# Optimization experiments

Hardware: AMD Instinct MI355X
Metric: run time of the kernel (lower is better)

The kernel has to match this reference:

```python
import jax, jax.numpy as jnp
import numpy as np
from jax import lax

WINDOW_SIZE = 11
SIGMA = 1.5
C1 = 0.01 ** 2
C2 = 0.03 ** 2


def _gaussian_window(channel, window_size, sigma=SIGMA):
    x = jnp.arange(window_size, dtype=jnp.float32)
    g = jnp.exp(-((x - window_size // 2) ** 2) / (2.0 * sigma * sigma))
    g = g / g.sum()
    w2d = jnp.outer(g, g)  # [ws, ws]
    # depthwise kernel in OIHW with feature_group_count=channel: [C, 1, ws, ws]
    return jnp.broadcast_to(w2d[None, None], (channel, 1, window_size, window_size))


def _dwconv(x, window, pad, channel):
    return lax.conv_general_dilated(
        x, window, window_strides=(1, 1), padding=[(pad, pad), (pad, pad)],
        dimension_numbers=("NCHW", "OIHW", "NCHW"), feature_group_count=channel)


def setup_inputs() -> dict:
    key = jax.random.key(0)
    k1, k2 = jax.random.split(key)
    shape = (16, 3, 512, 512)
    img1 = jax.random.uniform(k1, shape, dtype=jnp.float32)
    img2 = jax.random.uniform(k2, shape, dtype=jnp.float32)
    return {"img1": img1, "img2": img2}


def reference(img1, img2):
    _, channel, height, width = img1.shape
    ws = min(WINDOW_SIZE, height, width)
    window = _gaussian_window(channel, ws).astype(img1.dtype)
    pad = WINDOW_SIZE // 2  # matches torch code: padding=window_size // 2

    mu1 = _dwconv(img1, window, pad, channel)
    mu2 = _dwconv(img2, window, pad, channel)
    mu1_sq = mu1 * mu1
    mu2_sq = mu2 * mu2
    mu1_mu2 = mu1 * mu2

    sigma1_sq = _dwconv(img1 * img1, window, pad, channel) - mu1_sq
    sigma2_sq = _dwconv(img2 * img2, window, pad, channel) - mu2_sq
    sigma12 = _dwconv(img1 * img2, window, pad, channel) - mu1_mu2

    ssim_map = ((2.0 * mu1_mu2 + C1) * (2.0 * sigma12 + C2)) / (
        (mu1_sq + mu2_sq + C1) * (sigma1_sq + sigma2_sq + C2))
    return 1.0 - ssim_map.mean()
```

## Files before the change

### kernel.cpp

```cpp
#include <hip/hip_runtime.h>
#include <hip/hip_fp16.h>


#define IMGH 512
#define IMGW 512
#define TW 64
#define TH 32
#define GX 8
#define GY 16
#define GZ 48
#define NBLOCKS (GX * GY * GZ)
#define NPIX (16 * 3 * 512 * 512)
#define C1F 1.0e-4f
#define C2F 9.0e-4f

#define INSTRIDE 88
#define INPLANE (42 * INSTRIDE)
#define VSTRIDE 44
#define VPLANE (64 * VSTRIDE)
#define WBASE 34

#define W0 0.0010283818f
#define W1 0.0075987503f
#define W2 0.0360007547f
#define W3 0.1093606960f
#define W4 0.2130055367f
#define W5 0.2660117184f

typedef _Float16 half8v __attribute__((ext_vector_type(8)));
typedef float f32x4 __attribute__((ext_vector_type(4)));
union H8 { half8v v; __half2 h2[4]; float4 f4; unsigned u[4]; };

static __device__ __forceinline__ __half2 pkrtz(float a, float b) {
    auto r = __builtin_amdgcn_cvt_pkrtz(a, b);
    return *reinterpret_cast<__half2*>(&r);
}

__global__ __launch_bounds__(512, 8)
void ssim_tile(const float* __restrict__ img1, const float* __restrict__ img2,
               float* __restrict__ partials) {
    __shared__ _Float16 sWext[96];
    __shared__ _Float16 sIn[2 * INPLANE];
    __shared__ _Float16 sV[4 * VPLANE];
    __shared__ float wsum[8];

    const int tid  = threadIdx.x;
    const int lane = tid & 63;
    const int wv   = tid >> 6;
    const int lr = lane & 15;
    const int kc = lane >> 4;
    const int r0 = blockIdx.y * TH;
    const int c0 = blockIdx.x * TW;
    const size_t pbase = (size_t)blockIdx.z * (IMGH * IMGW);
    const float* a0 = img1 + pbase;
    const float* b0 = img2 + pbase;
    const bool fast = (blockIdx.x >= 1) & (blockIdx.x <= GX - 2) &
                      (blockIdx.y >= 1) & (blockIdx.y <= GY - 2);

    if (tid < 96) {
        const float W[11] = {W0, W1, W2, W3, W4, W5, W4, W3, W2, W1, W0};
        float w = 0.f;
#pragma unroll
        for (int j = 0; j < 11; ++j) w = (tid == WBASE + j) ? W[j] : w;
        sWext[tid] = (_Float16)w;
    }
    if (tid < 256) {
        const int q = tid >> 6, col = tid & 63;
        *reinterpret_cast<unsigned*>(&sV[q * VPLANE + col * VSTRIDE + 42]) = 0u;
    }

    if (tid < 420) {
        const int row = (unsigned)tid / 10u;
        const int ch  = tid - row * 10;
        const int gr = r0 - 5 + row;
        const int gc = c0 - 8 + 8 * ch;
        float4 va1, va2, vb1, vb2;
        if (fast) {
            const float* pa = a0 + (size_t)gr * IMGW + gc;
            const float* pb = b0 + (size_t)gr * IMGW + gc;
            va1 = *reinterpret_cast<const float4*>(pa);
            va2 = *reinterpret_cast<const float4*>(pa + 4);
            vb1 = *reinterpret_cast<const float4*>(pb);
            vb2 = *reinterpret_cast<const float4*>(pb + 4);
        } else {
            va1 = make_float4(0.f, 0.f, 0.f, 0.f);
            va2 = vb1 = vb2 = va1;
            if ((unsigned)gr < IMGH && (unsigned)gc < IMGW) {
                const float* pa = a0 + (size_t)gr * IMGW + gc;
                const float* pb = b0 + (size_t)gr * IMGW + gc;
                va1 = *reinterpret_cast<const float4*>(pa);
                va2 = *reinterpret_cast<const float4*>(pa + 4);
                vb1 = *reinterpret_cast<const float4*>(pb);
                vb2 = *reinterpret_cast<const float4*>(pb + 4);
            }
        }
        const int off = row * INSTRIDE + 8 * ch;
        H8 ha, hb;
        ha.h2[0] = pkrtz(va1.x, va1.y); ha.h2[1] = pkrtz(va1.z, va1.w);
        ha.h2[2] = pkrtz(va2.x, va2.y); ha.h2[3] = pkrtz(va2.z, va2.w);
        hb.h2[0] = pkrtz(vb1.x, vb1.y); hb.h2[1] = pkrtz(vb1.z, vb1.w);
        hb.h2[2] = pkrtz(vb2.x, vb2.y); hb.h2[3] = pkrtz(vb2.z, vb2.w);
        *reinterpret_cast<float4*>(&sIn[off]) = ha.f4;
        *reinterpret_cast<float4*>(&sIn[INPLANE + off]) = hb.f4;
    }
    __syncthreads();

    half8v Wh, Av0, Av1;
    {
        const int bi = (kc << 3) - lr + WBASE;
#pragma unroll
        for (int e = 0; e < 8; ++e) Wh[e]  = sWext[bi - 3 + e];
#pragma unroll
        for (int e = 0; e < 8; ++e) Av0[e] = sWext[bi + e];
#pragma unroll
        for (int e = 0; e < 8; ++e) Av1[e] = sWext[bi - 4 + e];
    }

    {
        const int ct = (wv >> 1) & 3;
        const int qp = wv & 1;
#pragma unroll
        for (int rt = 0; rt < 3; ++rt) {
            const int rb = (rt == 0) ? 0 : (rt == 1 ? 16 : 26);
            const int base = (rb + lr) * INSTRIDE + 16 * ct + (kc << 3);
            H8 fa, fb;
            fa.f4 = *reinterpret_cast<const float4*>(&sIn[base]);
            fb.f4 = *reinterpret_cast<const float4*>(&sIn[INPLANE + base]);
            H8 f0, f1;
            if (qp == 0) {
                f0 = fa; f1 = fb;
            } else {
#pragma unroll
                for (int t = 0; t < 4; ++t) {
                    f0.h2[t] = __hfma2(fa.h2[t], fa.h2[t],
                                       __hmul2(fb.h2[t], fb.h2[t]));
                    f1.h2[t] = __hmul2(fa.h2[t], fb.h2[t]);
                }
            }
            f32x4 d0 = {0.f, 0.f, 0.f, 0.f}, d1 = d0;
            d0 = __builtin_amdgcn_mfma_f32_16x16x32_f16(f0.v, Wh, d0, 0, 0, 0);
            d1 = __builtin_amdgcn_mfma_f32_16x16x32_f16(f1.v, Wh, d1, 0, 0, 0);
            const int p0 = qp * 2, p1 = qp * 2 + 1;
            const int vb = (16 * ct + lr) * VSTRIDE + rb + (kc << 2);
            uint2 s0, s1;
            __half2 h;
            h = pkrtz(d0[0], d0[1]); s0.x = *reinterpret_cast<unsigned*>(&h);
            h = pkrtz(d0[2], d0[3]); s0.y = *reinterpret_cast<unsigned*>(&h);
            h = pkrtz(d1[0], d1[1]); s1.x = *reinterpret_cast<unsigned*>(&h);
            h = pkrtz(d1[2], d1[3]); s1.y = *reinterpret_cast<unsigned*>(&h);
            if (rt < 2) {
                *reinterpret_cast<uint2*>(&sV[p0 * VPLANE + vb]) = s0;
                *reinterpret_cast<uint2*>(&sV[p1 * VPLANE + vb]) = s1;
            } else {
                unsigned* q0 = reinterpret_cast<unsigned*>(&sV[p0 * VPLANE + vb]);
                unsigned* q1 = reinterpret_cast<unsigned*>(&sV[p1 * VPLANE + vb]);
                q0[0] = s0.x; q0[1] = s0.y;
                q1[0] = s1.x; q1[1] = s1.y;
            }
        }
    }
    __syncthreads();

    float lsum = 0.f;
    {
        const int ct2 = wv & 3;
        const int rt2 = wv >> 2;
        const int w0 = rt2 ? 12 : 0;
        const half8v Avx = rt2 ? Av1 : Av0;
        const int vcol = 16 * ct2 + lr;
        const int vbase = vcol * VSTRIDE + w0 + (kc << 3);
        auto vread = [&](int q) -> half8v {
            const _Float16* p = &sV[q * VPLANE + vbase];
            H8 c;
            *reinterpret_cast<uint2*>(&c.u[0]) =
                *reinterpret_cast<const uint2*>(p);
            *reinterpret_cast<uint2*>(&c.u[2]) =
                *reinterpret_cast<const uint2*>(p + 4);
            return c.v;
        };
        f32x4 d0 = {0.f, 0.f, 0.f, 0.f}, d1 = d0, d2 = d0, d3 = d0;
        d0 = __builtin_amdgcn_mfma_f32_16x16x32_f16(Avx, vread(0), d0, 0, 0, 0);
        d1 = __builtin_amdgcn_mfma_f32_16x16x32_f16(Avx, vread(1), d1, 0, 0, 0);
        d2 = __builtin_amdgcn_mfma_f32_16x16x32_f16(Avx, vread(2), d2, 0, 0, 0);
        d3 = __builtin_amdgcn_mfma_f32_16x16x32_f16(Avx, vread(3), d3, 0, 0, 0);
#pragma unroll
        for (int r = 0; r < 4; ++r) {
            const float mu1 = d0[r], mu2 = d1[r], S = d2[r], eab = d3[r];
            const float mu11 = mu1 * mu1, mu22 = mu2 * mu2, mu12 = mu1 * mu2;
            const float s12 = eab - mu12;
            const float num = (2.f * mu12 + C1F) * (2.f * s12 + C2F);
            const float den = (mu11 + mu22 + C1F) * ((S - mu11 - mu22) + C2F);
            lsum += num * __builtin_amdgcn_rcpf(den);
        }
    }

#pragma unroll
    for (int off = 32; off > 0; off >>= 1) lsum += __shfl_down(lsum, off, 64);
    if (lane == 0) wsum[wv] = lsum;
    __syncthreads();
    if (tid == 0) {
        float t = 0.f;
#pragma unroll
        for (int w = 0; w < 8; ++w) t += wsum[w];
        partials[((size_t)blockIdx.z * GY + blockIdx.y) * GX + blockIdx.x] = t;
    }
}

__global__ __launch_bounds__(1024)
void ssim_reduce(const float* __restrict__ partials, float* __restrict__ out, int n) {
    __shared__ float lds[1024];
    float s = 0.f;
    for (int i = threadIdx.x; i < n; i += 1024) s += partials[i];
    lds[threadIdx.x] = s;
    __syncthreads();
    for (int off = 512; off > 0; off >>= 1) {
        if ((int)threadIdx.x < off) lds[threadIdx.x] += lds[threadIdx.x + off];
        __syncthreads();
    }
    if (threadIdx.x == 0) out[0] = 1.f - lds[0] / (float)NPIX;
}

extern "C" void kernel_launch(void* const* d_in, const int* in_sizes, int n_in,
                              void* d_out, int out_size, void* d_ws, size_t ws_size,
                              hipStream_t stream) {
    const float* img1 = (const float*)d_in[0];
    const float* img2 = (const float*)d_in[1];
    float* out = (float*)d_out;
    float* partials = (float*)d_ws;

    dim3 grid(GX, GY, GZ);
    ssim_tile<<<grid, 512, 0, stream>>>(img1, img2, partials);
    ssim_reduce<<<1, 1024, 0, stream>>>(partials, out, NBLOCKS);
}
```

Measured before the change: 41.31 us.

## Stage fp32 input tiles via direct global-to-LDS loads, convert to fp16 later

Replaces the register-staged global loads and early fp16 conversion with global_load_lds 16-byte transfers that write fp32 tiles straight into shared memory, with the fp16 packing moved into the horizontal MFMA stage. This is meant to remove VGPR round trips and the ds_write traffic of the staging step. The fp32 staging buffer doubles the LDS footprint, so the launch-bounds occupancy hint drops from 8 to 6. Edge blocks now need an extra zero-fill pass and barrier before loading.

```diff
diff --git a/kernel.cpp b/kernel.cpp
--- a/kernel.cpp
+++ b/kernel.cpp
@@ -14,8 +14,10 @@
 #define C1F 1.0e-4f
 #define C2F 9.0e-4f
 
-#define INSTRIDE 88
-#define INPLANE (42 * INSTRIDE)
+#define SROW 84
+#define SPLANE (42 * SROW)
+#define SPLANE_B (SPLANE * 4)
+#define STAGE_B (2 * SPLANE_B)
 #define VSTRIDE 44
 #define VPLANE (64 * VSTRIDE)
 #define WBASE 34
@@ -35,13 +37,18 @@
     auto r = __builtin_amdgcn_cvt_pkrtz(a, b);
     return *reinterpret_cast<__half2*>(&r);
 }
-
-__global__ __launch_bounds__(512, 8)
+static __device__ __forceinline__ void gload16(const void* g, void* l) {
+    __builtin_amdgcn_global_load_lds(
+        (const __attribute__((address_space(1))) void*)g,
+        (__attribute__((address_space(3))) void*)l, 16, 0, 0);
+}
+
+__global__ __launch_bounds__(512, 6)
 void ssim_tile(const float* __restrict__ img1, const float* __restrict__ img2,
                float* __restrict__ partials) {
+    __shared__ float sStage[2 * SPLANE];
+    __shared__ _Float16 sV[4 * VPLANE];
     __shared__ _Float16 sWext[96];
-    __shared__ _Float16 sIn[2 * INPLANE];
-    __shared__ _Float16 sV[4 * VPLANE];
     __shared__ float wsum[8];
 
     const int tid  = threadIdx.x;
@@ -57,6 +64,13 @@
     const bool fast = (blockIdx.x >= 1) & (blockIdx.x <= GX - 2) &
                       (blockIdx.y >= 1) & (blockIdx.y <= GY - 2);
 
+    if (!fast) {
+        const float4 z4 = make_float4(0.f, 0.f, 0.f, 0.f);
+        for (int t = tid; t < 2 * SPLANE / 4; t += 512)
+            reinterpret_cast<float4*>(sStage)[t] = z4;
+        __syncthreads();
+    }
+
     if (tid < 96) {
         const float W[11] = {W0, W1, W2, W3, W4, W5, W4, W3, W2, W1, W0};
         float w = 0.f;
@@ -69,39 +83,22 @@
         *reinterpret_cast<unsigned*>(&sV[q * VPLANE + col * VSTRIDE + 42]) = 0u;
     }
 
-    if (tid < 420) {
-        const int row = (unsigned)tid / 10u;
-        const int ch  = tid - row * 10;
-        const int gr = r0 - 5 + row;
-        const int gc = c0 - 8 + 8 * ch;
-        float4 va1, va2, vb1, vb2;
-        if (fast) {
-            const float* pa = a0 + (size_t)gr * IMGW + gc;
-            const float* pb = b0 + (size_t)gr * IMGW + gc;
-            va1 = *reinterpret_cast<const float4*>(pa);
-            va2 = *reinterpret_cast<const float4*>(pa + 4);
-            vb1 = *reinterpret_cast<const float4*>(pb);
-            vb2 = *reinterpret_cast<const float4*>(pb + 4);
-        } else {
-            va1 = make_float4(0.f, 0.f, 0.f, 0.f);
-            va2 = vb1 = vb2 = va1;
-            if ((unsigned)gr < IMGH && (unsigned)gc < IMGW) {
-                const float* pa = a0 + (size_t)gr * IMGW + gc;
-                const float* pb = b0 + (size_t)gr * IMGW + gc;
-                va1 = *reinterpret_cast<const float4*>(pa);
-                va2 = *reinterpret_cast<const float4*>(pa + 4);
-                vb1 = *reinterpret_cast<const float4*>(pb);
-                vb2 = *reinterpret_cast<const float4*>(pb + 4);
+    for (int i = wv; i < 28; i += 8) {
+        const int o = (i << 10) + (lane << 4);
+        if (o < STAGE_B) {
+            const int plane = o >= SPLANE_B;
+            const int po = o - plane * SPLANE_B;
+            const int row = (unsigned)po / 336u;
+            const int c4 = (po - row * 336) >> 4;
+            if (c4 < 20) {
+                const int gr = r0 - 5 + row;
+                const int gc = c0 - 8 + (c4 << 2);
+                if (fast || ((unsigned)gr < IMGH && (unsigned)gc < IMGW)) {
+                    const float* g = (plane ? b0 : a0) + (size_t)gr * IMGW + gc;
+                    gload16(g, reinterpret_cast<char*>(sStage) + (i << 10));
+                }
             }
         }
-        const int off = row * INSTRIDE + 8 * ch;
-        H8 ha, hb;
-        ha.h2[0] = pkrtz(va1.x, va1.y); ha.h2[1] = pkrtz(va1.z, va1.w);
-        ha.h2[2] = pkrtz(va2.x, va2.y); ha.h2[3] = pkrtz(va2.z, va2.w);
-        hb.h2[0] = pkrtz(vb1.x, vb1.y); hb.h2[1] = pkrtz(vb1.z, vb1.w);
-        hb.h2[2] = pkrtz(vb2.x, vb2.y); hb.h2[3] = pkrtz(vb2.z, vb2.w);
-        *reinterpret_cast<float4*>(&sIn[off]) = ha.f4;
-        *reinterpret_cast<float4*>(&sIn[INPLANE + off]) = hb.f4;
     }
     __syncthreads();
 
@@ -122,19 +119,25 @@
 #pragma unroll
         for (int rt = 0; rt < 3; ++rt) {
             const int rb = (rt == 0) ? 0 : (rt == 1 ? 16 : 26);
-            const int base = (rb + lr) * INSTRIDE + 16 * ct + (kc << 3);
-            H8 fa, fb;
-            fa.f4 = *reinterpret_cast<const float4*>(&sIn[base]);
-            fb.f4 = *reinterpret_cast<const float4*>(&sIn[INPLANE + base]);
+            const int fo = (rb + lr) * SROW + 16 * ct + (kc << 3);
+            float4 va1 = *reinterpret_cast<const float4*>(&sStage[fo]);
+            float4 va2 = *reinterpret_cast<const float4*>(&sStage[fo + 4]);
+            float4 vb1 = *reinterpret_cast<const float4*>(&sStage[SPLANE + fo]);
+            float4 vb2 = *reinterpret_cast<const float4*>(&sStage[SPLANE + fo + 4]);
+            H8 ha, hb;
+            ha.h2[0] = pkrtz(va1.x, va1.y); ha.h2[1] = pkrtz(va1.z, va1.w);
+            ha.h2[2] = pkrtz(va2.x, va2.y); ha.h2[3] = pkrtz(va2.z, va2.w);
+            hb.h2[0] = pkrtz(vb1.x, vb1.y); hb.h2[1] = pkrtz(vb1.z, vb1.w);
+            hb.h2[2] = pkrtz(vb2.x, vb2.y); hb.h2[3] = pkrtz(vb2.z, vb2.w);
             H8 f0, f1;
             if (qp == 0) {
-                f0 = fa; f1 = fb;
+                f0 = ha; f1 = hb;
             } else {
 #pragma unroll
                 for (int t = 0; t < 4; ++t) {
-                    f0.h2[t] = __hfma2(fa.h2[t], fa.h2[t],
-                                       __hmul2(fb.h2[t], fb.h2[t]));
-                    f1.h2[t] = __hmul2(fa.h2[t], fb.h2[t]);
+                    f0.h2[t] = __hfma2(ha.h2[t], ha.h2[t],
+                                       __hmul2(hb.h2[t], hb.h2[t]));
+                    f1.h2[t] = __hmul2(ha.h2[t], hb.h2[t]);
                 }
             }
             f32x4 d0 = {0.f, 0.f, 0.f, 0.f}, d1 = d0;
@@ -167,8 +170,7 @@
         const int rt2 = wv >> 2;
         const int w0 = rt2 ? 12 : 0;
         const half8v Avx = rt2 ? Av1 : Av0;
-        const int vcol = 16 * ct2 + lr;
-        const int vbase = vcol * VSTRIDE + w0 + (kc << 3);
+        const int vbase = (16 * ct2 + lr) * VSTRIDE + w0 + (kc << 3);
         auto vread = [&](int q) -> half8v {
             const _Float16* p = &sV[q * VPLANE + vbase];
             H8 c;
```

Result: slower. 52.18 us (+26.3%).
